# Kernel tuning notes

Measured on AMD Instinct MI355X. Metric: run time of the kernel, lower is better.

## Reference

```python
import jax, jax.numpy as jnp
import numpy as np

HIDDEN = 32
DN = ('NCHW', 'OIHW', 'NCHW')


def setup_inputs() -> dict:
    key = jax.random.key(0)
    ks = jax.random.split(key, 16)
    B = 32768
    s = lambda *sh: 1.0 / np.sqrt(np.prod(sh[1:]) if len(sh) > 1 else sh[0])
    inp = {
        'x': jax.random.normal(ks[0], (B, 12, 3, 4, 4), jnp.float32),
        'hour': jax.random.uniform(ks[1], (B, 1), jnp.float32),
        # ConvLSTM cell: Conv2d(3+32 -> 4*32, k=3, pad=1)
        'conv_w': jax.random.normal(ks[2], (4 * HIDDEN, 3 + HIDDEN, 3, 3), jnp.float32) * 0.05,
        'conv_b': jnp.zeros((4 * HIDDEN,), jnp.float32),
        # hour embedding: Linear(1,16) -> ReLU -> Linear(16,32)
        'he_w1': jax.random.normal(ks[3], (1, 16), jnp.float32),
        'he_b1': jnp.zeros((16,), jnp.float32),
        'he_w2': jax.random.normal(ks[4], (16, 32), jnp.float32) * 0.25,
        'he_b2': jnp.zeros((32,), jnp.float32),
        # decoder: Linear(544,256) -> ReLU -> Linear(256,128) -> ReLU -> Linear(128,30) -> Sigmoid
        'd_w1': jax.random.normal(ks[5], (32 * 4 * 4 + 32, 256), jnp.float32) * 0.04,
        'd_b1': jnp.zeros((256,), jnp.float32),
        'd_w2': jax.random.normal(ks[6], (256, 128), jnp.float32) * 0.06,
        'd_b2': jnp.zeros((128,), jnp.float32),
        'd_w3': jax.random.normal(ks[7], (128, 30), jnp.float32) * 0.09,
        'd_b3': jnp.zeros((30,), jnp.float32),
    }
    return inp


def _convlstm_scan(x, conv_w, conv_b):
    B, T, C, H, W = x.shape
    h0 = jnp.zeros((B, HIDDEN, H, W), x.dtype)
    c0 = jnp.zeros((B, HIDDEN, H, W), x.dtype)

    def step(carry, xt):
        h, c = carry
        inp = jnp.concatenate([xt, h], axis=1)  # [B, 3+32, 4, 4]
        gates = jax.lax.conv_general_dilated(
            inp, conv_w, (1, 1), 'SAME', dimension_numbers=DN)
        gates = gates + conv_b[None, :, None, None]
        i, f, o, g = jnp.split(gates, 4, axis=1)
        c_next = jax.nn.sigmoid(f) * c + jax.nn.sigmoid(i) * jnp.tanh(g)
        h_next = jax.nn.sigmoid(o) * jnp.tanh(c_next)
        return (h_next, c_next), None

    xs = jnp.swapaxes(x, 0, 1)  # [T, B, C, H, W]
    (h, c), _ = jax.lax.scan(step, (h0, c0), xs)
    return h


def reference(x, hour, conv_w, conv_b, he_w1, he_b1, he_w2, he_b2,
              d_w1, d_b1, d_w2, d_b2, d_w3, d_b3):
    B = x.shape[0]
    h = _convlstm_scan(x, conv_w, conv_b)            # [B, 32, 4, 4]
    spatial = h.reshape(B, -1)                        # [B, 512]
    hf = jax.nn.relu(hour @ he_w1 + he_b1) @ he_w2 + he_b2  # [B, 32]
    z = jnp.concatenate([spatial, hf], axis=1)        # [B, 544]
    z = jax.nn.relu(z @ d_w1 + d_b1)
    z = jax.nn.relu(z @ d_w2 + d_b2)                  # (dropout is identity in eval)
    out = jax.nn.sigmoid(z @ d_w3 + d_b3)
    return out.reshape(B, 10, 3)
```

## Files before the change

### kernel.cpp

```cpp
#include <hip/hip_runtime.h>

typedef _Float16 f16;
typedef _Float16 f16x4 __attribute__((ext_vector_type(4)));
typedef _Float16 f16x8 __attribute__((ext_vector_type(8)));
typedef float f32x2 __attribute__((ext_vector_type(2)));
typedef float f32x4 __attribute__((ext_vector_type(4)));

#define MFMA16(a, b, c) __builtin_amdgcn_mfma_f32_16x16x32_f16((a), (b), (c), 0, 0, 0)

__device__ __forceinline__ float rcp_(float x) { return __builtin_amdgcn_rcpf(x); }
__device__ __forceinline__ float sigm(float v) { return rcp_(1.0f + __expf(-v)); }
__device__ __forceinline__ float tanh_(float v) { return 1.0f - 2.0f * rcp_(__expf(2.0f * v) + 1.0f); }

#define XP 10368
#define WSO 11520
#define SMEMA 29952
#define NGRP 8192
#define GRID_REC 512

extern "C" __global__ __launch_bounds__(256, 2)
void hwq_rec(const float* __restrict__ gx, const float* __restrict__ ghour,
             const float* __restrict__ gcw, const float* __restrict__ gcb,
             const float* __restrict__ ghw1, const float* __restrict__ ghb1,
             const float* __restrict__ ghw2, const float* __restrict__ ghb2,
             f16* __restrict__ wz)
{
  __shared__ __align__(16) char smem[SMEMA];
  const int tid = threadIdx.x;
  const int lane = tid & 63;
  const int wv = tid >> 6;
  const int mg = wv & 1;
  const int ng = wv >> 1;
  const int lr = lane & 15;
  const int lk = lane >> 4;
  const int TOFF[9] = {0, 1, 2, 6, 7, 8, 12, 13, 14};
  const int pp0 = (lr >> 2) * 6 + (lr & 3);

  {
    float* za = (float*)smem;
    for (int i = tid; i < 2880; i += 256) za[i] = 0.0f;
    f16* axs = (f16*)(smem + WSO);
    for (int i = tid; i < 4096; i += 256) {
      int m = i >> 5, k = i & 31;
      int tau = k >> 2, sl = k & 3;
      int oc = ((m & 3) << 5) + (m >> 2);
      f16 v = (f16)0.0f;
      if (sl < 3) v = (f16)gcw[oc * 315 + sl * 9 + tau];
      else if (tau == 4) v = (f16)gcb[oc];
      axs[i] = v;
    }
    __syncthreads();
  }
  f16x8 Ax1[4], Ax2[4];
  {
    if (tid < 64) {
      int b = tid >> 4, p = tid & 15;
      int cell = ((p >> 2) + 1) * 6 + (p & 3) + 1;
      *(f16*)(smem + XP + b * 288 + cell * 8 + 6) = (f16)1.0f;
    }
    #pragma unroll
    for (int mt = 0; mt < 4; ++mt) {
      Ax1[mt] = *(const f16x8*)(smem + WSO + (mg * 64 + mt * 16 + lr) * 64 + lk * 16);
      int m = mg * 64 + mt * 16 + lr;
      int oc = ((m & 3) << 5) + (m >> 2);
      f16x8 f = {(f16)0, (f16)0, (f16)0, (f16)0, (f16)0, (f16)0, (f16)0, (f16)0};
      if (lk == 0) {
        f[0] = (f16)gcw[oc * 315 + 8];
        f[1] = (f16)gcw[oc * 315 + 17];
        f[2] = (f16)gcw[oc * 315 + 26];
      }
      Ax2[mt] = f;
    }
    __syncthreads();
  }
  f16x8 Ah[9][4];
  {
    f16* wst = (f16*)(smem + WSO);
    #pragma unroll
    for (int c = 0; c < 4; ++c) {
      for (int i = tid; i < 9216; i += 256) {
        int mrow = i / 288, rem = i - mrow * 288;
        int m = c * 32 + mrow;
        int oc = ((m & 3) << 5) + (m >> 2);
        wst[i] = (f16)gcw[oc * 315 + 27 + rem];
      }
      __syncthreads();
      if (mg == (c >> 1)) {
        #pragma unroll
        for (int mtl = 0; mtl < 2; ++mtl) {
          int mt = (c & 1) * 2 + mtl;
          #pragma unroll
          for (int tap = 0; tap < 9; ++tap) {
            f16x8 f;
            #pragma unroll
            for (int j = 0; j < 8; ++j)
              f[j] = wst[(mtl * 16 + lr) * 288 + (lk * 8 + j) * 9 + tap];
            Ah[tap][mt] = f;
          }
        }
      }
      __syncthreads();
    }
  }

  const int hb  = (ng * 2) * 2592 + pp0 * 72 + lk * 16;
  const int xpb = XP + (ng * 2) * 288 + pp0 * 8;
  const int wb  = (ng * 2) * 2592 + (pp0 + 7) * 72 + (mg * 16 + lk) * 2;
  const int xo0 = TOFF[2 * lk] * 8;
  const int xo1 = TOFF[2 * lk + 1] * 8;
  const bool stg = tid < 192;
  const int sb = tid / 48, srem = tid - sb * 48;
  const int sp = srem & 15, sic = srem >> 4;
  const int xdst = XP + sb * 288 + (((sp >> 2) + 1) * 6 + (sp & 3) + 1) * 8 + sic * 2;
  const int zb_ = tid >> 6, zc16 = (tid >> 2) & 15, zpart = tid & 3;
  const int zaddr = zb_ * 2592 + ((zc16 >> 2) * 6 + (zc16 & 3) + 7) * 72 + zpart * 16;

  for (int grp = blockIdx.x; grp < NGRP; grp += GRID_REC) {
    const int bg = grp << 2;
    const float* gxb = gx + (size_t)bg * 576;
    const float* xsrc = gxb + (size_t)sb * 576 + srem;

    {
      f32x2 z2 = {0.f, 0.f};
      *(f32x2*)(smem + zaddr) = z2;
      *(f32x2*)(smem + zaddr + 8) = z2;
    }
    if (stg) *(f16*)(smem + xdst) = (f16)xsrc[0];
    float cst[4][2];
    #pragma unroll
    for (int mt = 0; mt < 4; ++mt) { cst[mt][0] = 0.0f; cst[mt][1] = 0.0f; }
    __syncthreads();

    for (int t = 0; t < 12; ++t) {
      float xv = 0.0f;
      if (t < 11 && stg) xv = xsrc[(t + 1) * 48];

      f32x4 acc[4][2];
      #pragma unroll
      for (int mt = 0; mt < 4; ++mt)
        #pragma unroll
        for (int nt = 0; nt < 2; ++nt) { f32x4 z = {0.f, 0.f, 0.f, 0.f}; acc[mt][nt] = z; }

      #pragma unroll
      for (int tap = 0; tap < 9; ++tap) {
        const int to = TOFF[tap] * 72;
        #pragma unroll
        for (int nt = 0; nt < 2; ++nt) {
          f16x8 bf = *(const f16x8*)(smem + hb + nt * 2592 + to);
          #pragma unroll
          for (int mt = 0; mt < 4; ++mt)
            acc[mt][nt] = MFMA16(Ah[tap][mt], bf, acc[mt][nt]);
        }
      }
      #pragma unroll
      for (int nt = 0; nt < 2; ++nt) {
        const int base = xpb + nt * 288;
        f16x4 lo = *(const f16x4*)(smem + base + xo0);
        f16x4 hi = *(const f16x4*)(smem + base + xo1);
        f16x8 bf1 = __builtin_shufflevector(lo, hi, 0, 1, 2, 3, 4, 5, 6, 7);
        f16x4 l8 = *(const f16x4*)(smem + base + 112);
        f16x8 bf2 = __builtin_shufflevector(l8, l8, 0, 1, 2, 3, 0, 1, 2, 3);
        #pragma unroll
        for (int mt = 0; mt < 4; ++mt) {
          acc[mt][nt] = MFMA16(Ax1[mt], bf1, acc[mt][nt]);
          acc[mt][nt] = MFMA16(Ax2[mt], bf2, acc[mt][nt]);
        }
      }
      __syncthreads();

      #pragma unroll
      for (int mt = 0; mt < 4; ++mt) {
        #pragma unroll
        for (int nt = 0; nt < 2; ++nt) {
          float ig = sigm(acc[mt][nt][0]);
          float fg = sigm(acc[mt][nt][1]);
          float og = sigm(acc[mt][nt][2]);
          float gg = tanh_(acc[mt][nt][3]);
          float cn = fg * cst[mt][nt] + ig * gg;
          cst[mt][nt] = cn;
          f16 h = (f16)(og * tanh_(cn));
          if (t < 11) {
            *(f16*)(smem + wb + nt * 2592 + mt * 8) = h;
          } else {
            int ch = mg * 16 + mt * 4 + lk;
            wz[(size_t)(bg + ng * 2 + nt) * 544 + ch * 16 + lr] = h;
          }
        }
      }
      if (t < 11) {
        if (stg) *(f16*)(smem + xdst) = (f16)xv;
      } else if (tid < 128) {
        int b = tid >> 5, k2 = tid & 31;
        float h0 = ghour[bg + b];
        float a = ghb2[k2];
        #pragma unroll
        for (int ii = 0; ii < 16; ++ii) {
          float u = fmaxf(h0 * ghw1[ii] + ghb1[ii], 0.0f);
          a += u * ghw2[ii * 32 + k2];
        }
        wz[(size_t)(bg + b) * 544 + 512 + k2] = (f16)a;
      }
      __syncthreads();
    }
  }
}

extern "C" __global__ void hwq_prep(const float* __restrict__ gdw1,
                                    const float* __restrict__ gdw2,
                                    const float* __restrict__ gdw3,
                                    f16* __restrict__ w1t, f16* __restrict__ w2t,
                                    f16* __restrict__ w3t)
{
  int i0 = blockIdx.x * 256 + threadIdx.x;
  int stride = gridDim.x * 256;
  for (int idx = i0; idx < 139264; idx += stride) {
    int n = idx / 544, k = idx - n * 544;
    w1t[idx] = (f16)gdw1[k * 256 + n];
  }
  for (int idx = i0; idx < 32768; idx += stride) {
    int n = idx >> 8, k = idx & 255;
    w2t[idx] = (f16)gdw2[k * 128 + n];
  }
  for (int idx = i0; idx < 4096; idx += stride) {
    int n = idx >> 7, k = idx & 127;
    w3t[idx] = (n < 30) ? (f16)gdw3[k * 30 + n] : (f16)0.0f;
  }
}

extern "C" __global__ __launch_bounds__(256, 2)
void hwq_dec(const f16* __restrict__ wz, const f16* __restrict__ w1t,
             const f16* __restrict__ w2t, const f16* __restrict__ w3t,
             const float* __restrict__ gdb1, const float* __restrict__ gdb2,
             const float* __restrict__ gdb3, float* __restrict__ gout)
{
  __shared__ __align__(16) char smem[55296];
  f16* a1 = (f16*)smem;
  f16* a2 = (f16*)(smem + 35840);
  const int tid = threadIdx.x;
  const int lane = tid & 63;
  const int wv = tid >> 6;
  const int lr = lane & 15;
  const int lk = lane >> 4;
  const int s0 = blockIdx.x << 6;

  f32x4 acc1[4][4];
  #pragma unroll
  for (int nt = 0; nt < 4; ++nt) {
    float bb = gdb1[wv * 64 + nt * 16 + lr];
    f32x4 bv = {bb, bb, bb, bb};
    #pragma unroll
    for (int mt = 0; mt < 4; ++mt) acc1[mt][nt] = bv;
  }
  for (int kt = 0; kt < 17; ++kt) {
    f16x8 af[4];
    #pragma unroll
    for (int mt = 0; mt < 4; ++mt)
      af[mt] = *(const f16x8*)(wz + (size_t)(s0 + mt * 16 + lr) * 544 + kt * 32 + lk * 8);
    #pragma unroll
    for (int nt = 0; nt < 4; ++nt) {
      f16x8 bf = *(const f16x8*)(w1t + (size_t)(wv * 64 + nt * 16 + lr) * 544 + kt * 32 + lk * 8);
      #pragma unroll
      for (int mt = 0; mt < 4; ++mt)
        acc1[mt][nt] = MFMA16(af[mt], bf, acc1[mt][nt]);
    }
  }
  #pragma unroll
  for (int mt = 0; mt < 4; ++mt)
    #pragma unroll
    for (int nt = 0; nt < 4; ++nt) {
      int n = wv * 64 + nt * 16 + lr;
      #pragma unroll
      for (int r = 0; r < 4; ++r)
        a1[(mt * 16 + lk * 4 + r) * 280 + n] = (f16)fmaxf(acc1[mt][nt][r], 0.0f);
    }
  __syncthreads();

  f32x4 acc2[4][2];
  #pragma unroll
  for (int nt = 0; nt < 2; ++nt) {
    float bb = gdb2[wv * 32 + nt * 16 + lr];
    f32x4 bv = {bb, bb, bb, bb};
    #pragma unroll
    for (int mt = 0; mt < 4; ++mt) acc2[mt][nt] = bv;
  }
  for (int kt = 0; kt < 8; ++kt) {
    f16x8 af[4];
    #pragma unroll
    for (int mt = 0; mt < 4; ++mt)
      af[mt] = *(const f16x8*)(a1 + (mt * 16 + lr) * 280 + kt * 32 + lk * 8);
    #pragma unroll
    for (int nt = 0; nt < 2; ++nt) {
      f16x8 bf = *(const f16x8*)(w2t + (size_t)(wv * 32 + nt * 16 + lr) * 256 + kt * 32 + lk * 8);
      #pragma unroll
      for (int mt = 0; mt < 4; ++mt)
        acc2[mt][nt] = MFMA16(af[mt], bf, acc2[mt][nt]);
    }
  }
  __syncthreads();
  #pragma unroll
  for (int mt = 0; mt < 4; ++mt)
    #pragma unroll
    for (int nt = 0; nt < 2; ++nt) {
      int n = wv * 32 + nt * 16 + lr;
      #pragma unroll
      for (int r = 0; r < 4; ++r)
        a2[(mt * 16 + lk * 4 + r) * 152 + n] = (f16)fmaxf(acc2[mt][nt][r], 0.0f);
    }
  __syncthreads();

  if (wv < 2) {
    int n = wv * 16 + lr;
    float bb = (n < 30) ? gdb3[n] : 0.0f;
    f32x4 acc3[4];
    #pragma unroll
    for (int mt = 0; mt < 4; ++mt) { f32x4 bv = {bb, bb, bb, bb}; acc3[mt] = bv; }
    #pragma unroll
    for (int kt = 0; kt < 4; ++kt) {
      f16x8 bf = *(const f16x8*)(w3t + n * 128 + kt * 32 + lk * 8);
      #pragma unroll
      for (int mt = 0; mt < 4; ++mt) {
        f16x8 af = *(const f16x8*)(a2 + (mt * 16 + lr) * 152 + kt * 32 + lk * 8);
        acc3[mt] = MFMA16(af, bf, acc3[mt]);
      }
    }
    if (n < 30) {
      #pragma unroll
      for (int mt = 0; mt < 4; ++mt)
        #pragma unroll
        for (int r = 0; r < 4; ++r)
          gout[(size_t)(s0 + mt * 16 + lk * 4 + r) * 30 + n] = sigm(acc3[mt][r]);
    }
  }
}

typedef _Float16 f16x4m __attribute__((ext_vector_type(4)));
#define OFF_B 46080
#define SMEM_BYTES (46080 + 17408)

extern "C" __global__ __launch_bounds__(256, 1)
void hwq_fused_mono(const float* __restrict__ gx, const float* __restrict__ ghour,
               const float* __restrict__ gcw, const float* __restrict__ gcb,
               const float* __restrict__ ghw1, const float* __restrict__ ghb1,
               const float* __restrict__ ghw2, const float* __restrict__ ghb2,
               const float* __restrict__ gdw1, const float* __restrict__ gdb1,
               const float* __restrict__ gdw2, const float* __restrict__ gdb2,
               const float* __restrict__ gdw3, const float* __restrict__ gdb3,
               float* __restrict__ gout)
{
  __shared__ __align__(16) char smem[SMEM_BYTES];
  const int tid = threadIdx.x;
  const int lane = tid & 63;
  const int wv = tid >> 6;
  const int mg = wv & 1;
  const int ng = wv >> 1;
  const int lr = lane & 15;
  const int lk = lane >> 4;
  const int bg = blockIdx.x << 4;

  f16x8 Ah[9][4];
  {
    f16* wst = (f16*)(smem);
    #pragma unroll
    for (int c = 0; c < 2; ++c) {
      __syncthreads();
      for (int i = tid; i < 18432; i += 256) {
        int oc = i / 288, rem = i - oc * 288;
        wst[i] = (f16)gcw[(c * 64 + oc) * 315 + 27 + rem];
      }
      __syncthreads();
      #pragma unroll
      for (int g = 0; g < 2; ++g) {
        int ocl = g * 32 + mg * 16 + lr;
        #pragma unroll
        for (int tap = 0; tap < 9; ++tap) {
          f16x8 f;
          #pragma unroll
          for (int j = 0; j < 8; ++j)
            f[j] = wst[ocl * 288 + (lk * 8 + j) * 9 + tap];
          Ah[tap][c * 2 + g] = f;
        }
      }
    }
  }
  f16x8 Ax[4];
  {
    f16* xw = (f16*)(smem + OFF_B);
    __syncthreads();
    for (int i = tid; i < 3456; i += 256) {
      int oc = i / 27, rem = i - oc * 27;
      xw[i] = (f16)gcw[oc * 315 + rem];
    }
    __syncthreads();
    #pragma unroll
    for (int mt = 0; mt < 4; ++mt) {
      int oc = mt * 32 + mg * 16 + lr;
      f16x8 f;
      #pragma unroll
      for (int j = 0; j < 8; ++j) {
        int k = lk * 8 + j;
        int tap = (k * 11) >> 5;
        int ic = k - 3 * tap;
        f16 v = (f16)0.0f;
        if (k < 27) v = xw[oc * 27 + ic * 9 + tap];
        f[j] = v;
      }
      Ax[mt] = f;
    }
    __syncthreads();
  }

  float bias[4][4];
  #pragma unroll
  for (int mt = 0; mt < 4; ++mt)
    #pragma unroll
    for (int r = 0; r < 4; ++r)
      bias[mt][r] = gcb[mt * 32 + mg * 16 + lk * 4 + r];

  {
    float* za = (float*)smem;
    for (int i = tid; i < 11520; i += 256) za[i] = 0.0f;
    float* zb = (float*)(smem + OFF_B);
    for (int i = tid; i < 1152; i += 256) zb[i] = 0.0f;
    __syncthreads();
    for (int i = tid; i < 768; i += 256) {
      int b = i / 48, rem = i - b * 48;
      int pos = rem & 15;
      int ic = rem >> 4;
      int pp = (pos >> 2) * 6 + (pos & 3) + 7;
      *(f16*)(smem + OFF_B + b * 288 + pp * 8 + ic * 2) =
          (f16)gx[(size_t)(bg + b) * 576 + rem];
    }
    __syncthreads();
  }

  int hbase[8], xbase[8], wbase[8];
  #pragma unroll
  for (int nt = 0; nt < 8; ++nt) {
    int n = ng * 128 + nt * 16 + lr;
    int b = n >> 4, pos = n & 15;
    int pp0 = (pos >> 2) * 6 + (pos & 3);
    hbase[nt] = b * 2880 + pp0 * 80 + lk * 16;
    xbase[nt] = OFF_B + b * 288 + pp0 * 8;
    wbase[nt] = b * 2880 + (pp0 + 7) * 80 + (mg * 16 + lk * 4) * 2;
  }
  int xoff[8], xval[8];
  #pragma unroll
  for (int j = 0; j < 8; ++j) {
    int k = lk * 8 + j;
    int tap = (k * 11) >> 5;
    int ic = k - 3 * tap;
    xoff[j] = ((tap / 3) * 6 + (tap % 3)) * 8 + ic * 2;
    xval[j] = (k < 27);
  }

  const int TOFF[9] = {0, 1, 2, 6, 7, 8, 12, 13, 14};

  f32x4 cst[8];
  #pragma unroll
  for (int nt = 0; nt < 8; ++nt) { f32x4 z = {0.f, 0.f, 0.f, 0.f}; cst[nt] = z; }

  for (int t = 0; t < 12; ++t) {
    f32x4 acc[4][8];
    #pragma unroll
    for (int mt = 0; mt < 4; ++mt) {
      f32x4 bi = {bias[mt][0], bias[mt][1], bias[mt][2], bias[mt][3]};
      #pragma unroll
      for (int nt = 0; nt < 8; ++nt) acc[mt][nt] = bi;
    }
    #pragma unroll
    for (int tap = 0; tap < 9; ++tap) {
      #pragma unroll
      for (int nt = 0; nt < 8; ++nt) {
        f16x8 bf = *(const f16x8*)(smem + hbase[nt] + TOFF[tap] * 80);
        #pragma unroll
        for (int mt = 0; mt < 4; ++mt)
          acc[mt][nt] = MFMA16(Ah[tap][mt], bf, acc[mt][nt]);
      }
    }
    #pragma unroll
    for (int nt = 0; nt < 8; ++nt) {
      f16x8 bf;
      #pragma unroll
      for (int j = 0; j < 8; ++j) {
        int a = xval[j] ? (xbase[nt] + xoff[j]) : OFF_B;
        bf[j] = *(const f16*)(smem + a);
      }
      #pragma unroll
      for (int mt = 0; mt < 4; ++mt)
        acc[mt][nt] = MFMA16(Ax[mt], bf, acc[mt][nt]);
    }
    __syncthreads();

    #pragma unroll
    for (int nt = 0; nt < 8; ++nt) {
      f16 hh[4];
      #pragma unroll
      for (int r = 0; r < 4; ++r) {
        float ig = sigm(acc[0][nt][r]);
        float fg = sigm(acc[1][nt][r]);
        float og = sigm(acc[2][nt][r]);
        float gg = tanh_(acc[3][nt][r]);
        float cn = fg * cst[nt][r] + ig * gg;
        cst[nt][r] = cn;
        hh[r] = (f16)(og * tanh_(cn));
      }
      if (t < 11) {
        f16x4m hv = {hh[0], hh[1], hh[2], hh[3]};
        *(f16x4m*)(smem + wbase[nt]) = hv;
      } else {
        int n = ng * 128 + nt * 16 + lr;
        int b = n >> 4, pos = n & 15;
        int ch0 = mg * 16 + lk * 4;
        #pragma unroll
        for (int r = 0; r < 4; ++r)
          *(f16*)(smem + OFF_B + b * 1088 + (ch0 + r) * 32 + pos * 2) = hh[r];
      }
    }
    if (t < 11) {
      for (int i = tid; i < 768; i += 256) {
        int b = i / 48, rem = i - b * 48;
        int pos = rem & 15;
        int ic = rem >> 4;
        int pp = (pos >> 2) * 6 + (pos & 3) + 7;
        *(f16*)(smem + OFF_B + b * 288 + pp * 8 + ic * 2) =
            (f16)gx[(size_t)(bg + b) * 576 + (t + 1) * 48 + rem];
      }
    } else {
      for (int i = tid; i < 512; i += 256) {
        int b = i >> 5, k2 = i & 31;
        float h0 = ghour[bg + b];
        float a = ghb2[k2];
        #pragma unroll
        for (int ii = 0; ii < 16; ++ii) {
          float u = fmaxf(h0 * ghw1[ii] + ghb1[ii], 0.0f);
          a += u * ghw2[ii * 32 + k2];
        }
        *(f16*)(smem + OFF_B + b * 1088 + (512 + k2) * 2) = (f16)a;
      }
    }
    __syncthreads();
  }

  f16* zz  = (f16*)(smem + OFF_B);
  f16* wch = (f16*)(smem);
  f16* a1  = (f16*)(smem + 16384);
  f16* a2  = (f16*)(smem + 24576);
  f16* w3s = (f16*)(smem + 28672);

  f32x4 acc1[4];
  #pragma unroll
  for (int i = 0; i < 4; ++i) { f32x4 z = {0.f, 0.f, 0.f, 0.f}; acc1[i] = z; }
  for (int kt = 0; kt < 17; ++kt) {
    __syncthreads();
    for (int i = tid; i < 8192; i += 256) {
      int k = i >> 8, n = i & 255;
      wch[i] = (f16)gdw1[(kt * 32 + k) * 256 + n];
    }
    __syncthreads();
    f16x8 af = *(const f16x8*)((char*)zz + lr * 1088 + (kt * 32 + lk * 8) * 2);
    #pragma unroll
    for (int nt = 0; nt < 4; ++nt) {
      int n = (wv * 4 + nt) * 16 + lr;
      f16x8 bf;
      #pragma unroll
      for (int j = 0; j < 8; ++j) bf[j] = wch[(lk * 8 + j) * 256 + n];
      acc1[nt] = MFMA16(af, bf, acc1[nt]);
    }
  }
  __syncthreads();
  #pragma unroll
  for (int nt = 0; nt < 4; ++nt) {
    int n = (wv * 4 + nt) * 16 + lr;
    float bb = gdb1[n];
    #pragma unroll
    for (int r = 0; r < 4; ++r)
      a1[(lk * 4 + r) * 256 + n] = (f16)fmaxf(acc1[nt][r] + bb, 0.0f);
  }

  f32x4 acc2[2];
  #pragma unroll
  for (int i = 0; i < 2; ++i) { f32x4 z = {0.f, 0.f, 0.f, 0.f}; acc2[i] = z; }
  for (int kt = 0; kt < 8; ++kt) {
    __syncthreads();
    for (int i = tid; i < 4096; i += 256) {
      int k = i >> 7, n = i & 127;
      wch[i] = (f16)gdw2[(kt * 32 + k) * 128 + n];
    }
    __syncthreads();
    f16x8 af = *(const f16x8*)((char*)a1 + lr * 512 + (kt * 32 + lk * 8) * 2);
    #pragma unroll
    for (int nt = 0; nt < 2; ++nt) {
      int n = (wv * 2 + nt) * 16 + lr;
      f16x8 bf;
      #pragma unroll
      for (int j = 0; j < 8; ++j) bf[j] = wch[(lk * 8 + j) * 128 + n];
      acc2[nt] = MFMA16(af, bf, acc2[nt]);
    }
  }
  __syncthreads();
  #pragma unroll
  for (int nt = 0; nt < 2; ++nt) {
    int n = (wv * 2 + nt) * 16 + lr;
    float bb = gdb2[n];
    #pragma unroll
    for (int r = 0; r < 4; ++r)
      a2[(lk * 4 + r) * 128 + n] = (f16)fmaxf(acc2[nt][r] + bb, 0.0f);
  }
  __syncthreads();

  for (int i = tid; i < 4096; i += 256) {
    int k = i >> 5, n = i & 31;
    w3s[i] = (n < 30) ? (f16)gdw3[k * 30 + n] : (f16)0.0f;
  }
  __syncthreads();
  if (wv < 2) {
    f32x4 acc3 = {0.f, 0.f, 0.f, 0.f};
    int n = wv * 16 + lr;
    #pragma unroll
    for (int kt = 0; kt < 4; ++kt) {
      f16x8 af = *(const f16x8*)((char*)a2 + lr * 256 + (kt * 32 + lk * 8) * 2);
      f16x8 bf;
      #pragma unroll
      for (int j = 0; j < 8; ++j) bf[j] = w3s[(kt * 32 + lk * 8 + j) * 32 + n];
      acc3 = MFMA16(af, bf, acc3);
    }
    if (n < 30) {
      float bb = gdb3[n];
      #pragma unroll
      for (int r = 0; r < 4; ++r) {
        float v = sigm(acc3[r] + bb);
        gout[(size_t)(bg + lk * 4 + r) * 30 + n] = v;
      }
    }
  }
}

extern "C" void kernel_launch(void* const* d_in, const int* in_sizes, int n_in,
                              void* d_out, int out_size, void* d_ws, size_t ws_size,
                              hipStream_t stream) {
  (void)in_sizes; (void)n_in; (void)out_size;
  const size_t W1OFF = 35651584;
  const size_t W2OFF = W1OFF + 278528;
  const size_t W3OFF = W2OFF + 65536;
  const size_t NEED  = W3OFF + 8192;
  if (ws_size >= NEED) {
    f16* wzp = (f16*)d_ws;
    f16* w1t = (f16*)((char*)d_ws + W1OFF);
    f16* w2t = (f16*)((char*)d_ws + W2OFF);
    f16* w3t = (f16*)((char*)d_ws + W3OFF);
    hwq_prep<<<256, 256, 0, stream>>>((const float*)d_in[8], (const float*)d_in[10],
                                      (const float*)d_in[12], w1t, w2t, w3t);
    hwq_rec<<<GRID_REC, 256, 0, stream>>>(
        (const float*)d_in[0], (const float*)d_in[1], (const float*)d_in[2],
        (const float*)d_in[3], (const float*)d_in[4], (const float*)d_in[5],
        (const float*)d_in[6], (const float*)d_in[7], wzp);
    hwq_dec<<<512, 256, 0, stream>>>(wzp, w1t, w2t, w3t,
                                     (const float*)d_in[9], (const float*)d_in[11],
                                     (const float*)d_in[13], (float*)d_out);
  } else {
    hwq_fused_mono<<<2048, 256, 0, stream>>>(
        (const float*)d_in[0],  (const float*)d_in[1],  (const float*)d_in[2],
        (const float*)d_in[3],  (const float*)d_in[4],  (const float*)d_in[5],
        (const float*)d_in[6],  (const float*)d_in[7],  (const float*)d_in[8],
        (const float*)d_in[9],  (const float*)d_in[10], (const float*)d_in[11],
        (const float*)d_in[12], (const float*)d_in[13], (float*)d_out);
  }
}
```

Measured before the change: 714.1 us.

## Double-buffer LDS hidden state, drop mid-step barrier, fold log2e scaling into weights

Hidden-state and input tiles in LDS are now double-buffered by timestep parity, so the barrier between the MFMA reads and the gate writeback is removed and only one barrier per step remains. The cell stride is padded from 72 to 80 bytes, which may reduce LDS bank conflicts. Conv weights and bias are prescaled by -log2e (or 2·log2e for the g gate), so the gate activations use exp2 directly and the sigmoid·tanh output is merged into a single reciprocal. LDS use per block grows from about 30 KB to about 44 KB, and the algebraic rewrite changes rounding in fp16 weights.

```diff
diff --git a/kernel.cpp b/kernel.cpp
--- a/kernel.cpp
+++ b/kernel.cpp
@@ -11,10 +11,16 @@
 __device__ __forceinline__ float rcp_(float x) { return __builtin_amdgcn_rcpf(x); }
 __device__ __forceinline__ float sigm(float v) { return rcp_(1.0f + __expf(-v)); }
 __device__ __forceinline__ float tanh_(float v) { return 1.0f - 2.0f * rcp_(__expf(2.0f * v) + 1.0f); }
-
-#define XP 10368
-#define WSO 11520
-#define SMEMA 29952
+__device__ __forceinline__ float exp2_(float x) { return __builtin_amdgcn_exp2f(x); }
+
+#define LOG2E 1.4426950408889634f
+#define HCELL 80
+#define HSAMP 2880
+#define HBUFB 11520
+#define XP0 23040
+#define XBUFB 1152
+#define WSO 25344
+#define SMEMA 43776
 #define NGRP 8192
 #define GRID_REC 512
 
@@ -38,36 +44,38 @@
 
   {
     float* za = (float*)smem;
-    for (int i = tid; i < 2880; i += 256) za[i] = 0.0f;
+    for (int i = tid; i < 6336; i += 256) za[i] = 0.0f;
     f16* axs = (f16*)(smem + WSO);
     for (int i = tid; i < 4096; i += 256) {
       int m = i >> 5, k = i & 31;
       int tau = k >> 2, sl = k & 3;
       int oc = ((m & 3) << 5) + (m >> 2);
+      float sc = ((m & 3) == 3) ? (2.0f * LOG2E) : (-LOG2E);
       f16 v = (f16)0.0f;
-      if (sl < 3) v = (f16)gcw[oc * 315 + sl * 9 + tau];
-      else if (tau == 4) v = (f16)gcb[oc];
+      if (sl < 3) v = (f16)(sc * gcw[oc * 315 + sl * 9 + tau]);
+      else if (tau == 4) v = (f16)(sc * gcb[oc]);
       axs[i] = v;
     }
     __syncthreads();
   }
   f16x8 Ax1[4], Ax2[4];
   {
-    if (tid < 64) {
-      int b = tid >> 4, p = tid & 15;
+    if (tid < 128) {
+      int xb = tid >> 6, b = (tid >> 4) & 3, p = tid & 15;
       int cell = ((p >> 2) + 1) * 6 + (p & 3) + 1;
-      *(f16*)(smem + XP + b * 288 + cell * 8 + 6) = (f16)1.0f;
+      *(f16*)(smem + XP0 + xb * XBUFB + b * 288 + cell * 8 + 6) = (f16)1.0f;
     }
     #pragma unroll
     for (int mt = 0; mt < 4; ++mt) {
       Ax1[mt] = *(const f16x8*)(smem + WSO + (mg * 64 + mt * 16 + lr) * 64 + lk * 16);
       int m = mg * 64 + mt * 16 + lr;
       int oc = ((m & 3) << 5) + (m >> 2);
+      float sc = ((m & 3) == 3) ? (2.0f * LOG2E) : (-LOG2E);
       f16x8 f = {(f16)0, (f16)0, (f16)0, (f16)0, (f16)0, (f16)0, (f16)0, (f16)0};
       if (lk == 0) {
-        f[0] = (f16)gcw[oc * 315 + 8];
-        f[1] = (f16)gcw[oc * 315 + 17];
-        f[2] = (f16)gcw[oc * 315 + 26];
+        f[0] = (f16)(sc * gcw[oc * 315 + 8]);
+        f[1] = (f16)(sc * gcw[oc * 315 + 17]);
+        f[2] = (f16)(sc * gcw[oc * 315 + 26]);
       }
       Ax2[mt] = f;
     }
@@ -82,7 +90,8 @@
         int mrow = i / 288, rem = i - mrow * 288;
         int m = c * 32 + mrow;
         int oc = ((m & 3) << 5) + (m >> 2);
-        wst[i] = (f16)gcw[oc * 315 + 27 + rem];
+        float sc = ((m & 3) == 3) ? (2.0f * LOG2E) : (-LOG2E);
+        wst[i] = (f16)(sc * gcw[oc * 315 + 27 + rem]);
       }
       __syncthreads();
       if (mg == (c >> 1)) {
@@ -103,17 +112,17 @@
     }
   }
 
-  const int hb  = (ng * 2) * 2592 + pp0 * 72 + lk * 16;
-  const int xpb = XP + (ng * 2) * 288 + pp0 * 8;
-  const int wb  = (ng * 2) * 2592 + (pp0 + 7) * 72 + (mg * 16 + lk) * 2;
+  const int hb  = (ng * 2) * HSAMP + pp0 * HCELL + lk * 16;
+  const int xpb = XP0 + (ng * 2) * 288 + pp0 * 8;
+  const int wb  = (ng * 2) * HSAMP + (pp0 + 7) * HCELL + (mg * 16 + lk) * 2;
   const int xo0 = TOFF[2 * lk] * 8;
   const int xo1 = TOFF[2 * lk + 1] * 8;
   const bool stg = tid < 192;
   const int sb = tid / 48, srem = tid - sb * 48;
   const int sp = srem & 15, sic = srem >> 4;
-  const int xdst = XP + sb * 288 + (((sp >> 2) + 1) * 6 + (sp & 3) + 1) * 8 + sic * 2;
+  const int xdst = XP0 + sb * 288 + (((sp >> 2) + 1) * 6 + (sp & 3) + 1) * 8 + sic * 2;
   const int zb_ = tid >> 6, zc16 = (tid >> 2) & 15, zpart = tid & 3;
-  const int zaddr = zb_ * 2592 + ((zc16 >> 2) * 6 + (zc16 & 3) + 7) * 72 + zpart * 16;
+  const int zaddr = zb_ * HSAMP + ((zc16 >> 2) * 6 + (zc16 & 3) + 7) * HCELL + zpart * 16;
 
   for (int grp = blockIdx.x; grp < NGRP; grp += GRID_REC) {
     const int bg = grp << 2;
@@ -132,6 +141,8 @@
     __syncthreads();
 
     for (int t = 0; t < 12; ++t) {
+      const int rb  = (t & 1) * HBUFB;
+      const int xrb = (t & 1) * XBUFB;
       float xv = 0.0f;
       if (t < 11 && stg) xv = xsrc[(t + 1) * 48];
 
@@ -143,10 +154,10 @@
 
       #pragma unroll
       for (int tap = 0; tap < 9; ++tap) {
-        const int to = TOFF[tap] * 72;
+        const int to = rb + hb + TOFF[tap] * HCELL;
         #pragma unroll
         for (int nt = 0; nt < 2; ++nt) {
-          f16x8 bf = *(const f16x8*)(smem + hb + nt * 2592 + to);
+          f16x8 bf = *(const f16x8*)(smem + to + nt * HSAMP);
           #pragma unroll
           for (int mt = 0; mt < 4; ++mt)
             acc[mt][nt] = MFMA16(Ah[tap][mt], bf, acc[mt][nt]);
@@ -154,7 +165,7 @@
       }
       #pragma unroll
       for (int nt = 0; nt < 2; ++nt) {
-        const int base = xpb + nt * 288;
+        const int base = xrb + xpb + nt * 288;
         f16x4 lo = *(const f16x4*)(smem + base + xo0);
         f16x4 hi = *(const f16x4*)(smem + base + xo1);
         f16x8 bf1 = __builtin_shufflevector(lo, hi, 0, 1, 2, 3, 4, 5, 6, 7);
@@ -166,21 +177,25 @@
           acc[mt][nt] = MFMA16(Ax2[mt], bf2, acc[mt][nt]);
         }
       }
-      __syncthreads();
-
+
+      const int wbuf = HBUFB - rb;
       #pragma unroll
       for (int mt = 0; mt < 4; ++mt) {
         #pragma unroll
         for (int nt = 0; nt < 2; ++nt) {
-          float ig = sigm(acc[mt][nt][0]);
-          float fg = sigm(acc[mt][nt][1]);
-          float og = sigm(acc[mt][nt][2]);
-          float gg = tanh_(acc[mt][nt][3]);
-          float cn = fg * cst[mt][nt] + ig * gg;
+          float Ei = exp2_(acc[mt][nt][0]);
+          float Ef = exp2_(acc[mt][nt][1]);
+          float Eo = exp2_(acc[mt][nt][2]);
+          float Eg = exp2_(acc[mt][nt][3]);
+          float ig = rcp_(1.0f + Ei);
+          float fg = rcp_(1.0f + Ef);
+          float gs = 2.0f * LOG2E - (4.0f * LOG2E) * rcp_(1.0f + Eg);
+          float cn = fg * cst[mt][nt] + ig * gs;
           cst[mt][nt] = cn;
-          f16 h = (f16)(og * tanh_(cn));
+          float Ec = exp2_(cn);
+          f16 h = (f16)((Ec - 1.0f) * rcp_((1.0f + Eo) * (1.0f + Ec)));
           if (t < 11) {
-            *(f16*)(smem + wb + nt * 2592 + mt * 8) = h;
+            *(f16*)(smem + wbuf + wb + nt * HSAMP + mt * 8) = h;
           } else {
             int ch = mg * 16 + mt * 4 + lk;
             wz[(size_t)(bg + ng * 2 + nt) * 544 + ch * 16 + lr] = h;
@@ -188,7 +203,7 @@
         }
       }
       if (t < 11) {
-        if (stg) *(f16*)(smem + xdst) = (f16)xv;
+        if (stg) *(f16*)(smem + (XBUFB - xrb) + xdst) = (f16)xv;
       } else if (tid < 128) {
         int b = tid >> 5, k2 = tid & 31;
         float h0 = ghour[bg + b];
```

After: 677.6 us. 1.05x faster.
